# Optimization experiments

Measured on AMD Instinct MI355X. Metric: run time of the kernel, lower is better.

## Reference

```python
import jax, jax.numpy as jnp
import numpy as np

B, Q, D = 8, 128, 2048
H, HD = 16, 128           # num_heads, head_dim (D == H*HD)
CACHE = 3968              # tokens already in KV cache; CACHE+Q == max_seq_len


def setup_inputs() -> dict:
    key = jax.random.key(0)
    ks = jax.random.split(key, 6)
    x = jax.random.normal(ks[0], (B, Q, D), dtype=jnp.float32)
    k_cache = jax.random.normal(ks[1], (B, H, CACHE, HD), dtype=jnp.float32)
    v_cache = jax.random.normal(ks[2], (B, H, CACHE, HD), dtype=jnp.float32)
    Wqkv = jax.random.normal(ks[3], (D, 3 * D), dtype=jnp.float32) * 0.02
    Wproj = jax.random.normal(ks[4], (D, D), dtype=jnp.float32) * 0.02
    bproj = jnp.zeros((D,), dtype=jnp.float32)
    return {"x": x, "k_cache": k_cache, "v_cache": v_cache,
            "Wqkv": Wqkv, "Wproj": Wproj, "bproj": bproj}


def reference(x, k_cache, v_cache, Wqkv, Wproj, bproj):
    # QKV projection (qkv_bias=False)
    qkv = x @ Wqkv                                   # [B, Q, 3D]
    qkv = qkv.reshape(B, Q, 3, H, HD)
    qkv = jnp.transpose(qkv, (2, 0, 3, 1, 4))        # [3, B, H, Q, HD]
    q, k_new, v_new = qkv[0], qkv[1], qkv[2]
    # KV-cache append (cache_pos + Q == max_seq_len, no roll)
    k_all = jnp.concatenate([k_cache, k_new], axis=2)  # [B, H, K, HD]
    v_all = jnp.concatenate([v_cache, v_new], axis=2)
    K = CACHE + Q
    scale = 1.0 / jnp.sqrt(jnp.float32(HD))
    scores = jnp.einsum('bhqd,bhkd->bhqk', q, k_all) * scale  # [B, H, Q, K]
    # Causal mask aligned to cache (bottom-right): query i sees keys j <= i + (K - Q)
    i = jnp.arange(Q)[:, None]
    j = jnp.arange(K)[None, :]
    mask = j > (i + (K - Q))
    scores = jnp.where(mask, jnp.float32(-jnp.inf), scores)
    attn = jax.nn.softmax(scores, axis=-1)
    out = jnp.einsum('bhqk,bhkd->bhqd', attn, v_all)   # [B, H, Q, HD]
    out = jnp.transpose(out, (0, 2, 1, 3)).reshape(B, Q, D)
    return out @ Wproj + bproj
```

## Files before the change

### kernel.cpp

```cpp
#include <hip/hip_runtime.h>

typedef unsigned int u32;
typedef unsigned short u16;
typedef short s16x8 __attribute__((ext_vector_type(8)));
typedef float f32x4 __attribute__((ext_vector_type(4)));

#define MFMA16(a,b,c) __builtin_amdgcn_mfma_f32_16x16x32_bf16((a),(b),(c),0,0,0)

#define Bb 8
#define Hh 16
#define Qq 128
#define HDd 128
#define Dd 2048
#define CACHE 3968
#define NSPLIT 8
#define SCALE 0.08838834764831845f

__device__ __forceinline__ u16 f2bf(float x){
  u32 u = __builtin_bit_cast(u32, x);
  u32 r = ((u >> 16) & 1u) + 0x7fffu;
  return (u16)((u + r) >> 16);
}
__device__ __forceinline__ float bf2f(u16 h){
  return __builtin_bit_cast(float, ((u32)h) << 16);
}
__device__ __forceinline__ u32 pk2(float a, float b){
  return (u32)f2bf(a) | ((u32)f2bf(b) << 16);
}
__device__ __forceinline__ float f4c(const float4& v, int j){
  return j==0 ? v.x : j==1 ? v.y : j==2 ? v.z : v.w;
}
__device__ __forceinline__ void gload_lds16(const void* g, void* l){
  __builtin_amdgcn_global_load_lds(
      (const __attribute__((address_space(1))) u32*)g,
      (__attribute__((address_space(3))) u32*)l, 16, 0, 0);
}

__global__ void k_cvt(const float* __restrict__ s, u16* __restrict__ d, int n4){
  int i = blockIdx.x * 256 + threadIdx.x;
  if (i < n4){
    float4 v = *(const float4*)(s + (size_t)i * 4);
    *(uint2*)(d + (size_t)i * 4) = make_uint2(pk2(v.x, v.y), pk2(v.z, v.w));
  }
}

__global__ void k_tcvt(const float* __restrict__ s, u16* __restrict__ d, int R, int C){
  __shared__ float t[32][33];
  int tx = threadIdx.x & 31, ty = threadIdx.x >> 5;
  int c0 = blockIdx.x * 32, r0 = blockIdx.y * 32;
#pragma unroll
  for (int i = 0; i < 4; i++)
    t[ty + i*8][tx] = s[(size_t)(r0 + ty + i*8) * C + c0 + tx];
  __syncthreads();
#pragma unroll
  for (int i = 0; i < 4; i++)
    d[(size_t)(c0 + ty + i*8) * R + r0 + tx] = f2bf(t[tx][ty + i*8]);
}

template<int MODE>
__global__ __launch_bounds__(256)
void k_gemm(const u16* __restrict__ A, const u16* __restrict__ Bt, int K, int N,
            u16* __restrict__ oq, u16* __restrict__ ok, u16* __restrict__ ov,
            float* __restrict__ of, const float* __restrict__ bias)
{
  const int m0 = blockIdx.y * 128, n0 = blockIdx.x * 128;
  const int tid = threadIdx.x;
  const int w = tid >> 6, l = tid & 63;
  const int lg = l >> 4, lr = l & 15;
  const int wr = w >> 1, wc = w & 1;

  __shared__ u16 As[2][128 * 32];
  __shared__ u16 Bs[2][128 * 32];

  f32x4 acc[4][4];
#pragma unroll
  for (int i = 0; i < 4; i++)
#pragma unroll
    for (int j = 0; j < 4; j++) acc[i][j] = f32x4{0.f, 0.f, 0.f, 0.f};

  const int nt = K >> 5;

  auto stage = [&](int buf, int t){
    const int k0 = t << 5;
#pragma unroll
    for (int i = 0; i < 2; i++){
      int flat = i * 256 + tid;
      int row = flat >> 2, kq = flat & 3;
      const u16* ga = A + (size_t)(m0 + row) * K + k0 + kq * 8;
      gload_lds16(ga, (char*)&As[buf][0] + (size_t)(i*256 + w*64) * 16);
      const u16* gb = Bt + (size_t)(n0 + row) * K + k0 + kq * 8;
      gload_lds16(gb, (char*)&Bs[buf][0] + (size_t)(i*256 + w*64) * 16);
    }
  };

  stage(0, 0);
  asm volatile("s_waitcnt vmcnt(0)" ::: "memory");
  __syncthreads();

  for (int t = 0; t < nt; ++t){
    const int buf = t & 1;
    if (t + 1 < nt) stage(buf ^ 1, t + 1);
    s16x8 af[4], bfr[4];
#pragma unroll
    for (int i = 0; i < 4; i++){
      int row = wr*64 + i*16 + lr;
      af[i] = *(const s16x8*)&As[buf][row*32 + lg*8];
    }
#pragma unroll
    for (int j = 0; j < 4; j++){
      int col = wc*64 + j*16 + lr;
      bfr[j] = *(const s16x8*)&Bs[buf][col*32 + lg*8];
    }
#pragma unroll
    for (int i = 0; i < 4; i++)
#pragma unroll
      for (int j = 0; j < 4; j++)
        acc[i][j] = MFMA16(af[i], bfr[j], acc[i][j]);
    asm volatile("s_waitcnt vmcnt(0)" ::: "memory");
    __syncthreads();
  }

#pragma unroll
  for (int i = 0; i < 4; i++){
#pragma unroll
    for (int j = 0; j < 4; j++){
#pragma unroll
      for (int r = 0; r < 4; r++){
        int m = m0 + wr*64 + i*16 + lg*4 + r;
        int n = n0 + wc*64 + j*16 + lr;
        float v = acc[i][j][r];
        if (MODE == 0){
          int which = n >> 11;
          int h = (n >> 7) & 15, hd = n & 127;
          int b = m >> 7, qi = m & 127;
          size_t idx = (((size_t)(b * Hh + h)) * Qq + qi) * HDd + hd;
          if (which == 0)      oq[idx] = f2bf(v * SCALE);
          else if (which == 1) ok[idx] = f2bf(v);
          else                 ov[idx] = f2bf(v);
        } else {
          of[(size_t)m * N + n] = v + bias[n];
        }
      }
    }
  }
}

__global__ __launch_bounds__(512, 2)
void k_attn(const float* __restrict__ kc, const float* __restrict__ vc,
            const u16* __restrict__ qw, const u16* __restrict__ knw,
            const u16* __restrict__ vnw, float* __restrict__ opart,
            float2* __restrict__ ml)
{
  const int bh = blockIdx.x >> 3;
  const int sg = blockIdx.x & 7;
  const int tid = threadIdx.x;
  const int w = tid >> 6, l = tid & 63;
  const int lg = l >> 4, lr = l & 15;

  __shared__ u16 Ks[2][64 * 136];
  __shared__ u32 Vts[128 * 32];
  __shared__ u16 Pl[8 * 16 * 72];

  s16x8 qf[4];
  {
    const u16* qp = qw + (((size_t)bh * Qq + w*16 + lr) * HDd);
#pragma unroll
    for (int kk = 0; kk < 4; kk++) qf[kk] = *(const s16x8*)(qp + kk*32 + lg*8);
  }

  f32x4 acc[8];
#pragma unroll
  for (int i = 0; i < 8; i++) acc[i] = f32x4{0.f, 0.f, 0.f, 0.f};
  float mrow[4], lsum[4];
#pragma unroll
  for (int r = 0; r < 4; r++){ mrow[r] = -__builtin_inff(); lsum[r] = 0.f; }

  const float* kbase = kc + (size_t)bh * CACHE * HDd;
  const float* vbase = vc + (size_t)bh * CACHE * HDd;
  const u16* knb = knw + (size_t)bh * Qq * HDd;
  const u16* vnb = vnw + (size_t)bh * Qq * HDd;

  const int rv = tid & 15, c4v = tid >> 4;

  float4 kreg[4], vreg[4];

  auto loadc = [&](int c){
    if (c < 62){
#pragma unroll
      for (int i = 0; i < 4; i++){
        int flat = tid + i*512;
        int row = flat >> 5, c4 = flat & 31;
        kreg[i] = *(const float4*)(kbase + ((size_t)(c*64 + row)) * HDd + c4*4);
      }
#pragma unroll
      for (int a = 0; a < 4; a++)
        vreg[a] = *(const float4*)(vbase + ((size_t)(c*64 + rv + a*16)) * HDd + c4v*4);
    } else {
#pragma unroll
      for (int i = 0; i < 4; i++){
        int flat = tid + i*512;
        int row = flat >> 5, c4 = flat & 31;
        ushort4 u = *(const ushort4*)(knb + ((size_t)(c*64 + row - CACHE)) * HDd + c4*4);
        kreg[i] = make_float4(bf2f(u.x), bf2f(u.y), bf2f(u.z), bf2f(u.w));
      }
#pragma unroll
      for (int a = 0; a < 4; a++){
        ushort4 u = *(const ushort4*)(vnb + ((size_t)(c*64 + rv + a*16 - CACHE)) * HDd + c4v*4);
        vreg[a] = make_float4(bf2f(u.x), bf2f(u.y), bf2f(u.z), bf2f(u.w));
      }
    }
  };

  auto writeK = [&](int buf){
#pragma unroll
    for (int i = 0; i < 4; i++){
      int flat = tid + i*512;
      int row = flat >> 5, c4 = flat & 31;
      *(uint2*)&Ks[buf][row*136 + c4*4] =
          make_uint2(pk2(kreg[i].x, kreg[i].y), pk2(kreg[i].z, kreg[i].w));
    }
  };
  auto writeV = [&](){
#pragma unroll
    for (int j = 0; j < 4; j++){
      int col = c4v*4 + j;
      int x2 = (col & 7) << 2;
      Vts[col*32 + (rv ^ x2)]        = pk2(f4c(vreg[0], j), f4c(vreg[1], j));
      Vts[col*32 + ((rv + 16) ^ x2)] = pk2(f4c(vreg[2], j), f4c(vreg[3], j));
    }
  };

  int cur = 0;
  loadc(sg * 8);
  writeK(0);
  writeV();
  __syncthreads();

  for (int cl = 0; cl < 8; ++cl){
    const int c = sg * 8 + cl;
    if (cl + 1 < 8) loadc(c + 1);

    f32x4 s[4];
    __builtin_amdgcn_s_setprio(1);
#pragma unroll
    for (int t = 0; t < 4; t++){
      s[t] = f32x4{0.f, 0.f, 0.f, 0.f};
      const u16* kp = &Ks[cur][(t*16 + lr) * 136];
#pragma unroll
      for (int kk = 0; kk < 4; kk++){
        s16x8 kf = *(const s16x8*)(kp + kk*32 + lg*8);
        s[t] = MFMA16(qf[kk], kf, s[t]);
      }
    }
    __builtin_amdgcn_s_setprio(0);

    if (c >= 62){
      int jn = c*64 - CACHE;
#pragma unroll
      for (int t = 0; t < 4; t++){
        int kn = jn + t*16 + lr;
#pragma unroll
        for (int r = 0; r < 4; r++){
          int qi = w*16 + lg*4 + r;
          if (kn > qi) s[t][r] = -__builtin_inff();
        }
      }
    }
    float corr[4];
#pragma unroll
    for (int r = 0; r < 4; r++){
      float v = fmaxf(fmaxf(s[0][r], s[1][r]), fmaxf(s[2][r], s[3][r]));
      v = fmaxf(v, __shfl_xor(v, 1));
      v = fmaxf(v, __shfl_xor(v, 2));
      v = fmaxf(v, __shfl_xor(v, 4));
      v = fmaxf(v, __shfl_xor(v, 8));
      float mn = fmaxf(mrow[r], v);
      corr[r] = __expf(mrow[r] - mn);
      mrow[r] = mn;
    }
    float ps[4] = {0.f, 0.f, 0.f, 0.f};
#pragma unroll
    for (int t = 0; t < 4; t++)
#pragma unroll
      for (int r = 0; r < 4; r++){
        float p = __expf(s[t][r] - mrow[r]);
        s[t][r] = p;
        ps[r] += p;
      }
#pragma unroll
    for (int r = 0; r < 4; r++){
      float v = ps[r];
      v += __shfl_xor(v, 1);
      v += __shfl_xor(v, 2);
      v += __shfl_xor(v, 4);
      v += __shfl_xor(v, 8);
      lsum[r] = lsum[r] * corr[r] + v;
    }
#pragma unroll
    for (int i = 0; i < 8; i++)
#pragma unroll
      for (int r = 0; r < 4; r++) acc[i][r] *= corr[r];

    if (cl + 1 < 8) writeK(cur ^ 1);

    u16* pw = &Pl[w * 16 * 72];
#pragma unroll
    for (int r = 0; r < 4; r++){
      int row = lg*4 + r;
      *(u32*)&pw[row*72 + 2*lr]      = pk2(s[0][r], s[1][r]);
      *(u32*)&pw[row*72 + 32 + 2*lr] = pk2(s[2][r], s[3][r]);
    }
    s16x8 pf[2];
#pragma unroll
    for (int kk = 0; kk < 2; kk++)
      pf[kk] = *(const s16x8*)(pw + lr*72 + kk*32 + lg*8);

    __syncthreads();

    __builtin_amdgcn_s_setprio(1);
#pragma unroll
    for (int t = 0; t < 8; t++){
      int col = t*16 + lr;
      const u32* vp = &Vts[col * 32];
#pragma unroll
      for (int kk = 0; kk < 2; kk++){
        s16x8 vf = *(const s16x8*)(vp + ((16*kk + 4*lg) ^ ((col & 7) << 2)));
        acc[t] = MFMA16(pf[kk], vf, acc[t]);
      }
    }
    __builtin_amdgcn_s_setprio(0);

    __syncthreads();

    if (cl + 1 < 8) writeV();

    cur ^= 1;
  }

  float* pbase = opart + (size_t)blockIdx.x * (Qq * HDd);
#pragma unroll
  for (int t = 0; t < 8; t++){
#pragma unroll
    for (int r = 0; r < 4; r++){
      int qi = w*16 + lg*4 + r;
      pbase[(size_t)qi * HDd + t*16 + lr] = acc[t][r];
    }
  }
  if (lr == 0){
#pragma unroll
    for (int r = 0; r < 4; r++){
      int qi = w*16 + lg*4 + r;
      ml[(size_t)blockIdx.x * Qq + qi] = make_float2(mrow[r], lsum[r]);
    }
  }
}

__global__ __launch_bounds__(256)
void k_comb(const float* __restrict__ opart, const float2* __restrict__ ml,
            u16* __restrict__ ao)
{
  const int bh = blockIdx.x >> 2;
  const int q0 = (blockIdx.x & 3) * 32;
  const int tid = threadIdx.x;

  __shared__ float wgt[32][NSPLIT];
  __shared__ float Ls[32];

  {
    int row = tid >> 3, s = tid & 7;
    float2 v = ml[((size_t)(bh * NSPLIT + s)) * Qq + q0 + row];
    float m = v.x;
    m = fmaxf(m, __shfl_xor(m, 1));
    m = fmaxf(m, __shfl_xor(m, 2));
    m = fmaxf(m, __shfl_xor(m, 4));
    float e = __expf(v.x - m);
    float el = e * v.y;
    el += __shfl_xor(el, 1);
    el += __shfl_xor(el, 2);
    el += __shfl_xor(el, 4);
    wgt[row][s] = e;
    if (s == 0) Ls[row] = el;
  }
  __syncthreads();

  const int cp = tid & 63;
  const int r4 = tid >> 6;
  const int b = bh >> 4, h = bh & 15;
#pragma unroll
  for (int rr = 0; rr < 8; rr++){
    int row = r4 + rr*4;
    float2 a = make_float2(0.f, 0.f);
    const float* pb = opart + ((size_t)(bh * NSPLIT)) * (Qq * HDd)
                            + (size_t)(q0 + row) * HDd + cp*2;
#pragma unroll
    for (int s = 0; s < NSPLIT; s++){
      float2 p = *(const float2*)(pb + (size_t)s * (Qq * HDd));
      float wv = wgt[row][s];
      a.x += wv * p.x;
      a.y += wv * p.y;
    }
    float inv = 1.0f / Ls[row];
    u16* dst = ao + ((size_t)b * Qq + q0 + row) * Dd + h * HDd + cp*2;
    *(u32*)dst = pk2(a.x * inv, a.y * inv);
  }
}

extern "C" void kernel_launch(void* const* d_in, const int* in_sizes, int n_in,
                              void* d_out, int out_size, void* d_ws, size_t ws_size,
                              hipStream_t stream)
{
  const float* x     = (const float*)d_in[0];
  const float* kc    = (const float*)d_in[1];
  const float* vc    = (const float*)d_in[2];
  const float* wqkv  = (const float*)d_in[3];
  const float* wproj = (const float*)d_in[4];
  const float* bproj = (const float*)d_in[5];
  float* out = (float*)d_out;

  char* ws = (char*)d_ws;
  u16* xb  = (u16*)(ws);
  u16* wtq = (u16*)(ws + ((size_t)4  << 20));
  u16* wtp = (u16*)(ws + ((size_t)28 << 20));
  u16* qw  = (u16*)(ws + ((size_t)36 << 20));
  u16* knw = (u16*)(ws + ((size_t)40 << 20));
  u16* vnw = (u16*)(ws + ((size_t)44 << 20));
  u16* aow = (u16*)(ws + ((size_t)48 << 20));
  float* opart = (float*)(ws + ((size_t)52 << 20));
  float2* mlw  = (float2*)(ws + ((size_t)116 << 20));

  k_cvt<<<2048, 256, 0, stream>>>(x, xb, (1024 * 2048) / 4);
  k_tcvt<<<dim3(192, 64), 256, 0, stream>>>(wqkv, wtq, 2048, 6144);
  k_tcvt<<<dim3(64, 64), 256, 0, stream>>>(wproj, wtp, 2048, 2048);
  k_gemm<0><<<dim3(48, 8), 256, 0, stream>>>(xb, wtq, 2048, 6144,
                                             qw, knw, vnw, nullptr, nullptr);
  k_attn<<<Bb * Hh * NSPLIT, 512, 0, stream>>>(kc, vc, qw, knw, vnw, opart, mlw);
  k_comb<<<Bb * Hh * 4, 256, 0, stream>>>(opart, mlw, aow);
  k_gemm<1><<<dim3(16, 8), 256, 0, stream>>>(aow, wtp, 2048, 2048,
                                             nullptr, nullptr, nullptr, out, bproj);
}
```

Before: 293.6 us.

## Transpose attention MFMA operands so each lane owns one query row

Swaps the A/B operands of both MFMAs so the score and output accumulators are transposed, giving each lane a single query row. Row max and row sum then need two cross-lane shuffles instead of four reductions over four rows, and the running max/sum state shrinks to scalars. P is written to LDS as swizzled 16-byte vectors, and the partial outputs are staged through LDS so global stores are coalesced float4. The LDS staging adds two extra block barriers in the epilogue.

```diff
diff --git a/kernel.cpp b/kernel.cpp
--- a/kernel.cpp
+++ b/kernel.cpp
@@ -157,9 +157,9 @@
   const int w = tid >> 6, l = tid & 63;
   const int lg = l >> 4, lr = l & 15;
 
-  __shared__ u16 Ks[2][64 * 136];
+  __shared__ __align__(16) u16 Ks[2][64 * 136];
   __shared__ u32 Vts[128 * 32];
-  __shared__ u16 Pl[8 * 16 * 72];
+  __shared__ __align__(16) u16 Pl[8 * 16 * 72];
 
   s16x8 qf[4];
   {
@@ -171,9 +171,7 @@
   f32x4 acc[8];
 #pragma unroll
   for (int i = 0; i < 8; i++) acc[i] = f32x4{0.f, 0.f, 0.f, 0.f};
-  float mrow[4], lsum[4];
-#pragma unroll
-  for (int r = 0; r < 4; r++){ mrow[r] = -__builtin_inff(); lsum[r] = 0.f; }
+  float mrow = -__builtin_inff(), lsum = 0.f;
 
   const float* kbase = kc + (size_t)bh * CACHE * HDd;
   const float* vbase = vc + (size_t)bh * CACHE * HDd;
@@ -249,71 +247,66 @@
 #pragma unroll
       for (int kk = 0; kk < 4; kk++){
         s16x8 kf = *(const s16x8*)(kp + kk*32 + lg*8);
-        s[t] = MFMA16(qf[kk], kf, s[t]);
+        s[t] = MFMA16(kf, qf[kk], s[t]);
       }
     }
     __builtin_amdgcn_s_setprio(0);
 
     if (c >= 62){
       int jn = c*64 - CACHE;
-#pragma unroll
-      for (int t = 0; t < 4; t++){
-        int kn = jn + t*16 + lr;
+      int qi = w*16 + lr;
+#pragma unroll
+      for (int t = 0; t < 4; t++)
 #pragma unroll
         for (int r = 0; r < 4; r++){
-          int qi = w*16 + lg*4 + r;
+          int kn = jn + t*16 + lg*4 + r;
           if (kn > qi) s[t][r] = -__builtin_inff();
         }
-      }
-    }
-    float corr[4];
-#pragma unroll
-    for (int r = 0; r < 4; r++){
-      float v = fmaxf(fmaxf(s[0][r], s[1][r]), fmaxf(s[2][r], s[3][r]));
-      v = fmaxf(v, __shfl_xor(v, 1));
-      v = fmaxf(v, __shfl_xor(v, 2));
-      v = fmaxf(v, __shfl_xor(v, 4));
-      v = fmaxf(v, __shfl_xor(v, 8));
-      float mn = fmaxf(mrow[r], v);
-      corr[r] = __expf(mrow[r] - mn);
-      mrow[r] = mn;
-    }
-    float ps[4] = {0.f, 0.f, 0.f, 0.f};
+    }
+
+    float pmax = s[0][0];
 #pragma unroll
     for (int t = 0; t < 4; t++)
 #pragma unroll
+      for (int r = 0; r < 4; r++) pmax = fmaxf(pmax, s[t][r]);
+    pmax = fmaxf(pmax, __shfl_xor(pmax, 16));
+    pmax = fmaxf(pmax, __shfl_xor(pmax, 32));
+    float mn = fmaxf(mrow, pmax);
+    float corr = __expf(mrow - mn);
+    mrow = mn;
+    float ps = 0.f;
+#pragma unroll
+    for (int t = 0; t < 4; t++)
+#pragma unroll
       for (int r = 0; r < 4; r++){
-        float p = __expf(s[t][r] - mrow[r]);
+        float p = __expf(s[t][r] - mn);
         s[t][r] = p;
-        ps[r] += p;
-      }
-#pragma unroll
-    for (int r = 0; r < 4; r++){
-      float v = ps[r];
-      v += __shfl_xor(v, 1);
-      v += __shfl_xor(v, 2);
-      v += __shfl_xor(v, 4);
-      v += __shfl_xor(v, 8);
-      lsum[r] = lsum[r] * corr[r] + v;
-    }
+        ps += p;
+      }
+    ps += __shfl_xor(ps, 16);
+    ps += __shfl_xor(ps, 32);
+    lsum = lsum * corr + ps;
 #pragma unroll
     for (int i = 0; i < 8; i++)
 #pragma unroll
-      for (int r = 0; r < 4; r++) acc[i][r] *= corr[r];
+      for (int r = 0; r < 4; r++) acc[i][r] *= corr;
 
     if (cl + 1 < 8) writeK(cur ^ 1);
 
-    u16* pw = &Pl[w * 16 * 72];
-#pragma unroll
-    for (int r = 0; r < 4; r++){
-      int row = lg*4 + r;
-      *(u32*)&pw[row*72 + 2*lr]      = pk2(s[0][r], s[1][r]);
-      *(u32*)&pw[row*72 + 32 + 2*lr] = pk2(s[2][r], s[3][r]);
+    u16* pw = &Pl[(w*16 + lr) * 72];
+    {
+      int pl = lg ^ (lr & 3);
+      uint4 w01 = make_uint4(pk2(s[0][0], s[1][0]), pk2(s[0][1], s[1][1]),
+                             pk2(s[0][2], s[1][2]), pk2(s[0][3], s[1][3]));
+      uint4 w23 = make_uint4(pk2(s[2][0], s[3][0]), pk2(s[2][1], s[3][1]),
+                             pk2(s[2][2], s[3][2]), pk2(s[2][3], s[3][3]));
+      *(uint4*)((char*)pw + (pl << 4))       = w01;
+      *(uint4*)((char*)pw + ((4 + pl) << 4)) = w23;
     }
     s16x8 pf[2];
 #pragma unroll
     for (int kk = 0; kk < 2; kk++)
-      pf[kk] = *(const s16x8*)(pw + lr*72 + kk*32 + lg*8);
+      pf[kk] = *(const s16x8*)((char*)pw + ((kk*4 + (lg ^ (lr & 3))) << 4));
 
     __syncthreads();
 
@@ -325,7 +318,7 @@
 #pragma unroll
       for (int kk = 0; kk < 2; kk++){
         s16x8 vf = *(const s16x8*)(vp + ((16*kk + 4*lg) ^ ((col & 7) << 2)));
-        acc[t] = MFMA16(pf[kk], vf, acc[t]);
+        acc[t] = MFMA16(vf, pf[kk], acc[t]);
       }
     }
     __builtin_amdgcn_s_setprio(0);
@@ -338,21 +331,31 @@
   }
 
   float* pbase = opart + (size_t)blockIdx.x * (Qq * HDd);
-#pragma unroll
-  for (int t = 0; t < 8; t++){
-#pragma unroll
-    for (int r = 0; r < 4; r++){
-      int qi = w*16 + lg*4 + r;
-      pbase[(size_t)qi * HDd + t*16 + lr] = acc[t][r];
-    }
-  }
-  if (lr == 0){
-#pragma unroll
-    for (int r = 0; r < 4; r++){
-      int qi = w*16 + lg*4 + r;
-      ml[(size_t)blockIdx.x * Qq + qi] = make_float2(mrow[r], lsum[r]);
-    }
-  }
+  float* Lt = (float*)Ks;
+#pragma unroll 1
+  for (int half = 0; half < 2; half++){
+    if ((w >> 2) == half){
+      int ql = (w & 3) * 16 + lr;
+#pragma unroll
+      for (int t = 0; t < 8; t++)
+#pragma unroll
+        for (int r = 0; r < 4; r++)
+          Lt[ql * 132 + t*16 + lg*4 + r] = acc[t][r];
+    }
+    __syncthreads();
+    {
+      int c32 = tid & 31;
+#pragma unroll
+      for (int j = 0; j < 4; j++){
+        int ql = (tid >> 5) + j * 16;
+        float4 v = *(const float4*)&Lt[ql * 132 + c32 * 4];
+        *(float4*)&pbase[(size_t)(half * 64 + ql) * HDd + c32 * 4] = v;
+      }
+    }
+    __syncthreads();
+  }
+  if (lg == 0)
+    ml[(size_t)blockIdx.x * Qq + w*16 + lr] = make_float2(mrow, lsum);
 }
 
 __global__ __launch_bounds__(256)
```

Result: no change. 290.3 us (-1.1%).
